# Kernel optimization log

Hardware: AMD Instinct MI355X
Metric: run time of the kernel (lower is better)

## Reference

```python
import jax, jax.numpy as jnp
import numpy as np

N_NODES = 100000


def setup_inputs() -> dict:
    key = jax.random.key(0)
    k1, k2, k3 = jax.random.split(key, 3)
    x = jax.random.normal(k1, (N_NODES, 128), dtype=jnp.float32)
    edge_index = jax.random.randint(k2, (2, 1600000), 0, N_NODES, dtype=jnp.int64)
    # TAGConv K=1 linear weight: maps concat([x, Ax]) (2*in) -> out; stored as [(K+1)*in, out]
    W = (jax.random.normal(k3, (256, 128), dtype=jnp.float32) / np.sqrt(256.0)).astype(jnp.float32)
    return {"x": x, "edge_index": edge_index, "W": W}


def reference(x, edge_index, W):
    src, dst = edge_index[0], edge_index[1]
    n = x.shape[0]
    ones = jnp.ones(src.shape[0], dtype=x.dtype)
    # gcn_norm without self-loops: degree from edge weights scattered at target
    deg = jax.ops.segment_sum(ones, dst, num_segments=n)
    dis = jnp.where(deg > 0, jax.lax.rsqrt(jnp.where(deg > 0, deg, 1.0)), 0.0)
    norm = dis[src] * dis[dst]  # [E]
    # message passing: out[dst] += norm * x[src]
    msgs = x[src] * norm[:, None]  # [E, in]
    agg = jax.ops.segment_sum(msgs, dst, num_segments=n)  # [N, in]
    h = jnp.concatenate([x, agg], axis=1)  # [N, 2*in]
    return h @ W  # [N, out]
```

## Files before the change

### kernel.cpp

```cpp
#include <hip/hip_runtime.h>


#define GCN_F 128

typedef __attribute__((ext_vector_type(8))) short frag_ab;
typedef __attribute__((ext_vector_type(4))) float frag_cd;

__device__ __forceinline__ unsigned short f2bf(float f) {
    unsigned int u = __float_as_uint(f);
    unsigned int r = (u + 0x7FFFu + ((u >> 16) & 1u)) >> 16;
    return (unsigned short)r;
}

__global__ __launch_bounds__(256) void prep_kernel(const unsigned int* __restrict__ ei32,
                                                   const float* __restrict__ W,
                                                   unsigned short* __restrict__ wt,
                                                   int* __restrict__ flag) {
    if (blockIdx.x == 128) {
        unsigned int v = 0;
        for (int i = threadIdx.x; i < 4096; i += 256) v |= ei32[2 * i + 1];
        if (v != 0u) atomicOr(flag, 1);
        return;
    }
    int c = blockIdx.x;
    int k = threadIdx.x;
    wt[c * 256 + k] = f2bf(W[k * GCN_F + c]);
}

__device__ __forceinline__ int load_idx(const int* ei, int is32, long long pos) {
    if (is32) return ei[pos];
    return ((const int2*)ei)[pos].x;
}

__global__ __launch_bounds__(256) void chist_kernel(const int* __restrict__ ei,
                                                    const int* __restrict__ flag,
                                                    int* __restrict__ ccnt, int E) {
    __shared__ int h[256];
    int tid = threadIdx.x;
    h[tid] = 0;
    __syncthreads();
    int is32 = *flag;
    int base = blockIdx.x * 4096;
    for (int j = 0; j < 16; ++j) {
        int e = base + j * 256 + tid;
        if (e < E) {
            int dst = load_idx(ei, is32, (long long)E + e);
            atomicAdd(&h[dst >> 9], 1);
        }
    }
    __syncthreads();
    if (h[tid]) atomicAdd(&ccnt[tid], h[tid]);
}

__global__ __launch_bounds__(256) void cscan_kernel(const int* __restrict__ ccnt,
                                                    int* __restrict__ cs,
                                                    int* __restrict__ ccur) {
    __shared__ int tmp[256];
    int tid = threadIdx.x;
    int v = ccnt[tid];
    tmp[tid] = v;
    __syncthreads();
    for (int off = 1; off < 256; off <<= 1) {
        int t = (tid >= off) ? tmp[tid - off] : 0;
        __syncthreads();
        tmp[tid] += t;
        __syncthreads();
    }
    int ex = tmp[tid] - v;
    cs[tid] = ex;
    ccur[tid] = ex;
    if (tid == 255) cs[256] = tmp[255];
}

__global__ __launch_bounds__(256) void cscatter_kernel(const int* __restrict__ ei,
                                                       const int* __restrict__ flag,
                                                       int* __restrict__ ccur,
                                                       unsigned int* __restrict__ epack,
                                                       int E) {
    __shared__ int h[256];
    __shared__ int lcur[256];
    int tid = threadIdx.x;
    h[tid] = 0;
    __syncthreads();
    int is32 = *flag;
    int base = blockIdx.x * 4096;
    unsigned int pk[16];
    int bn[16];
#pragma unroll
    for (int j = 0; j < 16; ++j) {
        int e = base + j * 256 + tid;
        bn[j] = -1;
        pk[j] = 0;
        if (e < E) {
            int src = load_idx(ei, is32, e);
            int dst = load_idx(ei, is32, (long long)E + e);
            pk[j] = (unsigned int)src | (((unsigned int)dst & 511u) << 17);
            bn[j] = dst >> 9;
            atomicAdd(&h[bn[j]], 1);
        }
    }
    __syncthreads();
    {
        int cnt = h[tid];
        lcur[tid] = (cnt > 0) ? atomicAdd(&ccur[tid], cnt) : 0;
    }
    __syncthreads();
#pragma unroll
    for (int j = 0; j < 16; ++j) {
        if (bn[j] >= 0) {
            int pos = atomicAdd(&lcur[bn[j]], 1);
            epack[pos] = pk[j];
        }
    }
}

__global__ __launch_bounds__(512) void fcsr_kernel(const unsigned int* __restrict__ epack,
                                                   const int* __restrict__ cs,
                                                   int* __restrict__ start,
                                                   float* __restrict__ dis,
                                                   int* __restrict__ ebuf,
                                                   int N, int E) {
    __shared__ int lh[512];
    __shared__ int sc[512];
    int c = blockIdx.x;
    int tid = threadIdx.x;
    lh[tid] = 0;
    __syncthreads();
    int b = cs[c], e = cs[c + 1];
    for (int i = b + tid; i < e; i += 512) {
        atomicAdd(&lh[(epack[i] >> 17) & 511u], 1);
    }
    __syncthreads();
    sc[tid] = lh[tid];
    __syncthreads();
    for (int off = 1; off < 512; off <<= 1) {
        int t = (tid >= off) ? sc[tid - off] : 0;
        __syncthreads();
        sc[tid] += t;
        __syncthreads();
    }
    int d = lh[tid];
    int gs = b + sc[tid] - d;
    int node = c * 512 + tid;
    if (node < N) {
        start[node] = gs;
        dis[node] = (d > 0) ? rsqrtf((float)d) : 0.0f;
    }
    __syncthreads();
    sc[tid] = gs;
    if (c == 0 && tid == 0) start[N] = E;
    __syncthreads();
    for (int i = b + tid; i < e; i += 512) {
        unsigned int v = epack[i];
        int pos = atomicAdd(&sc[(v >> 17) & 511u], 1);
        ebuf[pos] = (int)(v & 0x1FFFFu);
    }
}

__global__ __launch_bounds__(256) void xbf_kernel(const float4* __restrict__ x4,
                                                  unsigned short* __restrict__ h, int N) {
    int g = blockIdx.x * 256 + threadIdx.x;
    if (g >= N * 32) return;
    int r = g >> 5, q = g & 31;
    float4 v = x4[(long long)r * 32 + q];
    ushort4 o;
    o.x = f2bf(v.x); o.y = f2bf(v.y); o.z = f2bf(v.z); o.w = f2bf(v.w);
    *(ushort4*)(h + (long long)r * 256 + q * 4) = o;
}

__global__ __launch_bounds__(256) void gather_kernel(unsigned short* __restrict__ h,
                                                     const int* __restrict__ ebuf,
                                                     const int* __restrict__ start,
                                                     const float* __restrict__ dis,
                                                     int N) {
    int node = blockIdx.x * 4 + (threadIdx.x >> 6);
    if (node >= N) return;
    int lane = threadIdx.x & 63;
    int slot = lane >> 4;
    int sub  = lane & 15;
    int s = start[node];
    int d = start[node + 1] - s;
    float acc[8];
#pragma unroll
    for (int i = 0; i < 8; ++i) acc[i] = 0.0f;

    for (int base = 0; base < d; base += 64) {
        int cn = min(64, d - base);
        int eid = 0; float dv = 0.0f;
        if (lane < cn) {
            eid = ebuf[s + base + lane];
            dv = dis[eid];
        }
        int njj = (cn + 3) >> 2;
#pragma unroll 4
        for (int j = 0; j < njj; ++j) {
            int tt = 4 * j + slot;
            int src = __shfl(eid, tt);
            float f = __shfl(dv, tt);
            uint4 u = *(const uint4*)(h + (long long)src * 256 + sub * 8);
            acc[0] += f * __uint_as_float(u.x << 16);
            acc[1] += f * __uint_as_float(u.x);
            acc[2] += f * __uint_as_float(u.y << 16);
            acc[3] += f * __uint_as_float(u.y);
            acc[4] += f * __uint_as_float(u.z << 16);
            acc[5] += f * __uint_as_float(u.z);
            acc[6] += f * __uint_as_float(u.w << 16);
            acc[7] += f * __uint_as_float(u.w);
        }
    }
#pragma unroll
    for (int i = 0; i < 8; ++i) {
        acc[i] += __shfl_xor(acc[i], 16);
        acc[i] += __shfl_xor(acc[i], 32);
    }
    if (slot == 0) {
        float nd = dis[node];
        uint4 o;
        o.x = (unsigned int)f2bf(acc[0] * nd) | ((unsigned int)f2bf(acc[1] * nd) << 16);
        o.y = (unsigned int)f2bf(acc[2] * nd) | ((unsigned int)f2bf(acc[3] * nd) << 16);
        o.z = (unsigned int)f2bf(acc[4] * nd) | ((unsigned int)f2bf(acc[5] * nd) << 16);
        o.w = (unsigned int)f2bf(acc[6] * nd) | ((unsigned int)f2bf(acc[7] * nd) << 16);
        *(uint4*)(h + (long long)node * 256 + 128 + sub * 8) = o;
    }
}

#define GEMM_BM 128
__global__ __launch_bounds__(256) void gemm_mfma_kernel(
        const unsigned short* h,
        const unsigned short* __restrict__ wt,
        float* out, int N) {
    int wave = threadIdx.x >> 6;
    int lane = threadIdx.x & 63;
    int lr = lane & 15;
    int kh = lane >> 4;
    int rowbase = blockIdx.x * GEMM_BM + wave * 32;

    frag_cd acc[2][8];
#pragma unroll
    for (int rt = 0; rt < 2; ++rt)
#pragma unroll
        for (int ct = 0; ct < 8; ++ct) acc[rt][ct] = (frag_cd)0.0f;

    for (int ks = 0; ks < 8; ++ks) {
        frag_ab a[2];
#pragma unroll
        for (int rt = 0; rt < 2; ++rt) {
            int r = rowbase + rt * 16 + lr;
            r = min(r, N - 1);
            a[rt] = *(const frag_ab*)(h + (long long)r * 256 + ks * 32 + kh * 8);
        }
#pragma unroll
        for (int ct = 0; ct < 8; ++ct) {
            int c = ct * 16 + lr;
            frag_ab b = *(const frag_ab*)(wt + c * 256 + ks * 32 + kh * 8);
#pragma unroll
            for (int rt = 0; rt < 2; ++rt) {
                acc[rt][ct] = __builtin_amdgcn_mfma_f32_16x16x32_bf16(a[rt], b, acc[rt][ct], 0, 0, 0);
            }
        }
    }
#pragma unroll
    for (int rt = 0; rt < 2; ++rt) {
#pragma unroll
        for (int ct = 0; ct < 8; ++ct) {
#pragma unroll
            for (int reg = 0; reg < 4; ++reg) {
                int r = rowbase + rt * 16 + kh * 4 + reg;
                if (r < N) out[(long long)r * GCN_F + ct * 16 + lr] = acc[rt][ct][reg];
            }
        }
    }
}

extern "C" void kernel_launch(void* const* d_in, const int* in_sizes, int n_in,
                              void* d_out, int out_size, void* d_ws, size_t ws_size,
                              hipStream_t stream) {
    const float* x  = (const float*)d_in[0];
    const int*   ei = (const int*)d_in[1];
    const float* W  = (const float*)d_in[2];
    float* out = (float*)d_out;

    const int N = in_sizes[0] / GCN_F;
    const int E = in_sizes[1] / 2;

    char* ws = (char*)d_ws;
    int*   flag  = (int*)ws;
    int*   ccnt  = (int*)(ws + 1024);
    int*   cs    = (int*)(ws + 3072);
    int*   ccur  = (int*)(ws + 5120);
    float* dis   = (float*)(ws + 8192);
    int*   start = (int*)(ws + 408192);
    int*   ebuf  = (int*)(ws + 808208);
    unsigned short* wt = (unsigned short*)(ws + 7208208);

    unsigned int*   epack = (unsigned int*)d_out;
    unsigned short* h     = (unsigned short*)d_out;

    const int CB = (N + 511) / 512;
    const int EB = (E + 4095) / 4096;

    hipMemsetAsync(d_ws, 0, 2048, stream);

    prep_kernel<<<129, 256, 0, stream>>>((const unsigned int*)ei, W, wt, flag);
    chist_kernel<<<EB, 256, 0, stream>>>(ei, flag, ccnt, E);
    cscan_kernel<<<1, 256, 0, stream>>>(ccnt, cs, ccur);
    cscatter_kernel<<<EB, 256, 0, stream>>>(ei, flag, ccur, epack, E);
    fcsr_kernel<<<CB, 512, 0, stream>>>(epack, cs, start, dis, ebuf, N, E);
    xbf_kernel<<<(N * 32 + 255) / 256, 256, 0, stream>>>((const float4*)x, h, N);
    gather_kernel<<<(N + 3) / 4, 256, 0, stream>>>(h, ebuf, start, dis, N);
    gemm_mfma_kernel<<<(N + GEMM_BM - 1) / GEMM_BM, 256, 0, stream>>>(h, wt, out, N);
}
```

Measured before the change: 185.2 us.

## Fold prep work into histogram and CSR kernels, overlapping bf16 conversion

Drops the separate prep kernel. The W transpose now runs as extra blocks of the histogram kernel, and each block detects int32 vs int64 indices locally instead of through a global flag, which also shrinks the memset. The x-to-bf16 conversion is split: rows past the region that aliases the epack scratch are converted by extra blocks of the fcsr kernel, and only the low rows wait for a separate kernel after fcsr. It also adds per-wave shared histograms and 32-bit address arithmetic. The hard-coded 12500-row split assumes the epack size for E=1.6M edges, so other edge counts would corrupt data.

```diff
diff --git a/kernel.cpp b/kernel.cpp
--- a/kernel.cpp
+++ b/kernel.cpp
@@ -12,19 +12,14 @@
     return (unsigned short)r;
 }
 
-__global__ __launch_bounds__(256) void prep_kernel(const unsigned int* __restrict__ ei32,
-                                                   const float* __restrict__ W,
-                                                   unsigned short* __restrict__ wt,
-                                                   int* __restrict__ flag) {
-    if (blockIdx.x == 128) {
-        unsigned int v = 0;
-        for (int i = threadIdx.x; i < 4096; i += 256) v |= ei32[2 * i + 1];
-        if (v != 0u) atomicOr(flag, 1);
-        return;
-    }
-    int c = blockIdx.x;
-    int k = threadIdx.x;
-    wt[c * 256 + k] = f2bf(W[k * GCN_F + c]);
+__device__ __forceinline__ int detect_is32(const unsigned int* ei32, int* s_is32) {
+    if (threadIdx.x == 0) *s_is32 = 0;
+    __syncthreads();
+    unsigned int v = 0;
+    for (int i = threadIdx.x; i < 2048; i += blockDim.x) v |= ei32[2 * i + 1];
+    if (v != 0u) atomicOr(s_is32, 1);
+    __syncthreads();
+    return *s_is32;
 }
 
 __device__ __forceinline__ int load_idx(const int* ei, int is32, long long pos) {
@@ -33,23 +28,32 @@
 }
 
 __global__ __launch_bounds__(256) void chist_kernel(const int* __restrict__ ei,
-                                                    const int* __restrict__ flag,
-                                                    int* __restrict__ ccnt, int E) {
-    __shared__ int h[256];
+                                                    int* __restrict__ ccnt, int E, int EB,
+                                                    const float* __restrict__ W,
+                                                    unsigned short* __restrict__ wt) {
+    if ((int)blockIdx.x >= EB) {
+        int c = blockIdx.x - EB;
+        int k = threadIdx.x;
+        wt[c * 256 + k] = f2bf(W[k * GCN_F + c]);
+        return;
+    }
+    __shared__ int h[4][256];
+    __shared__ int s_is32;
     int tid = threadIdx.x;
-    h[tid] = 0;
-    __syncthreads();
-    int is32 = *flag;
+    int wv = tid >> 6;
+    for (int i = tid; i < 1024; i += 256) ((int*)h)[i] = 0;
+    int is32 = detect_is32((const unsigned int*)ei, &s_is32);
     int base = blockIdx.x * 4096;
     for (int j = 0; j < 16; ++j) {
         int e = base + j * 256 + tid;
         if (e < E) {
             int dst = load_idx(ei, is32, (long long)E + e);
-            atomicAdd(&h[dst >> 9], 1);
-        }
-    }
-    __syncthreads();
-    if (h[tid]) atomicAdd(&ccnt[tid], h[tid]);
+            atomicAdd(&h[wv][dst >> 9], 1);
+        }
+    }
+    __syncthreads();
+    int s = h[0][tid] + h[1][tid] + h[2][tid] + h[3][tid];
+    if (s) atomicAdd(&ccnt[tid], s);
 }
 
 __global__ __launch_bounds__(256) void cscan_kernel(const int* __restrict__ ccnt,
@@ -73,16 +77,15 @@
 }
 
 __global__ __launch_bounds__(256) void cscatter_kernel(const int* __restrict__ ei,
-                                                       const int* __restrict__ flag,
                                                        int* __restrict__ ccur,
                                                        unsigned int* __restrict__ epack,
                                                        int E) {
     __shared__ int h[256];
     __shared__ int lcur[256];
+    __shared__ int s_is32;
     int tid = threadIdx.x;
     h[tid] = 0;
-    __syncthreads();
-    int is32 = *flag;
+    int is32 = detect_is32((const unsigned int*)ei, &s_is32);
     int base = blockIdx.x * 4096;
     unsigned int pk[16];
     int bn[16];
@@ -119,11 +122,25 @@
                                                    int* __restrict__ start,
                                                    float* __restrict__ dis,
                                                    int* __restrict__ ebuf,
-                                                   int N, int E) {
+                                                   const float4* __restrict__ x4,
+                                                   unsigned short* __restrict__ hbuf,
+                                                   int N, int E, int CB) {
+    int tid = threadIdx.x;
+    if ((int)blockIdx.x >= CB) {
+        int chunk = blockIdx.x - CB;
+        int g = 12500 * 32 + chunk * 512 + tid;
+        if (g < N * 32) {
+            int r = g >> 5, q = g & 31;
+            float4 v = x4[(long long)r * 32 + q];
+            ushort4 o;
+            o.x = f2bf(v.x); o.y = f2bf(v.y); o.z = f2bf(v.z); o.w = f2bf(v.w);
+            *(ushort4*)((char*)hbuf + ((unsigned)r << 9) + q * 8) = o;
+        }
+        return;
+    }
     __shared__ int lh[512];
     __shared__ int sc[512];
     int c = blockIdx.x;
-    int tid = threadIdx.x;
     lh[tid] = 0;
     __syncthreads();
     int b = cs[c], e = cs[c + 1];
@@ -157,18 +174,18 @@
     }
 }
 
-__global__ __launch_bounds__(256) void xbf_kernel(const float4* __restrict__ x4,
-                                                  unsigned short* __restrict__ h, int N) {
+__global__ __launch_bounds__(256) void xbf_lo_kernel(const float4* __restrict__ x4,
+                                                     unsigned short* __restrict__ hbuf) {
     int g = blockIdx.x * 256 + threadIdx.x;
-    if (g >= N * 32) return;
+    if (g >= 12500 * 32) return;
     int r = g >> 5, q = g & 31;
     float4 v = x4[(long long)r * 32 + q];
     ushort4 o;
     o.x = f2bf(v.x); o.y = f2bf(v.y); o.z = f2bf(v.z); o.w = f2bf(v.w);
-    *(ushort4*)(h + (long long)r * 256 + q * 4) = o;
-}
-
-__global__ __launch_bounds__(256) void gather_kernel(unsigned short* __restrict__ h,
+    *(ushort4*)((char*)hbuf + ((unsigned)r << 9) + q * 8) = o;
+}
+
+__global__ __launch_bounds__(256) void gather_kernel(unsigned short* __restrict__ hbuf,
                                                      const int* __restrict__ ebuf,
                                                      const int* __restrict__ start,
                                                      const float* __restrict__ dis,
@@ -177,9 +194,11 @@
     if (node >= N) return;
     int lane = threadIdx.x & 63;
     int slot = lane >> 4;
-    int sub  = lane & 15;
+    unsigned int subb = (lane & 15) * 16;
     int s = start[node];
     int d = start[node + 1] - s;
+    float nd = dis[node];
+    const char* hc = (const char*)hbuf;
     float acc[8];
 #pragma unroll
     for (int i = 0; i < 8; ++i) acc[i] = 0.0f;
@@ -197,7 +216,7 @@
             int tt = 4 * j + slot;
             int src = __shfl(eid, tt);
             float f = __shfl(dv, tt);
-            uint4 u = *(const uint4*)(h + (long long)src * 256 + sub * 8);
+            uint4 u = *(const uint4*)(hc + (((unsigned)src << 9) + subb));
             acc[0] += f * __uint_as_float(u.x << 16);
             acc[1] += f * __uint_as_float(u.x);
             acc[2] += f * __uint_as_float(u.y << 16);
@@ -214,13 +233,12 @@
         acc[i] += __shfl_xor(acc[i], 32);
     }
     if (slot == 0) {
-        float nd = dis[node];
         uint4 o;
         o.x = (unsigned int)f2bf(acc[0] * nd) | ((unsigned int)f2bf(acc[1] * nd) << 16);
         o.y = (unsigned int)f2bf(acc[2] * nd) | ((unsigned int)f2bf(acc[3] * nd) << 16);
         o.z = (unsigned int)f2bf(acc[4] * nd) | ((unsigned int)f2bf(acc[5] * nd) << 16);
         o.w = (unsigned int)f2bf(acc[6] * nd) | ((unsigned int)f2bf(acc[7] * nd) << 16);
-        *(uint4*)(h + (long long)node * 256 + 128 + sub * 8) = o;
+        *(uint4*)((char*)hbuf + (((unsigned)node << 9) + 256 + subb)) = o;
     }
 }
 
@@ -234,6 +252,7 @@
     int lr = lane & 15;
     int kh = lane >> 4;
     int rowbase = blockIdx.x * GEMM_BM + wave * 32;
+    const char* hc = (const char*)h;
 
     frag_cd acc[2][8];
 #pragma unroll
@@ -247,7 +266,7 @@
         for (int rt = 0; rt < 2; ++rt) {
             int r = rowbase + rt * 16 + lr;
             r = min(r, N - 1);
-            a[rt] = *(const frag_ab*)(h + (long long)r * 256 + ks * 32 + kh * 8);
+            a[rt] = *(const frag_ab*)(hc + (((unsigned)r << 9) + (unsigned)(ks * 64 + kh * 16)));
         }
 #pragma unroll
         for (int ct = 0; ct < 8; ++ct) {
@@ -266,7 +285,7 @@
 #pragma unroll
             for (int reg = 0; reg < 4; ++reg) {
                 int r = rowbase + rt * 16 + kh * 4 + reg;
-                if (r < N) out[(long long)r * GCN_F + ct * 16 + lr] = acc[rt][ct][reg];
+                if (r < N) out[r * GCN_F + ct * 16 + lr] = acc[rt][ct][reg];
             }
         }
     }
@@ -284,10 +303,9 @@
     const int E = in_sizes[1] / 2;
 
     char* ws = (char*)d_ws;
-    int*   flag  = (int*)ws;
-    int*   ccnt  = (int*)(ws + 1024);
-    int*   cs    = (int*)(ws + 3072);
-    int*   ccur  = (int*)(ws + 5120);
+    int*   ccnt  = (int*)ws;
+    int*   cs    = (int*)(ws + 1024);
+    int*   ccur  = (int*)(ws + 3072);
     float* dis   = (float*)(ws + 8192);
     int*   start = (int*)(ws + 408192);
     int*   ebuf  = (int*)(ws + 808208);
@@ -298,15 +316,17 @@
 
     const int CB = (N + 511) / 512;
     const int EB = (E + 4095) / 4096;
-
-    hipMemsetAsync(d_ws, 0, 2048, stream);
-
-    prep_kernel<<<129, 256, 0, stream>>>((const unsigned int*)ei, W, wt, flag);
-    chist_kernel<<<EB, 256, 0, stream>>>(ei, flag, ccnt, E);
+    const int XBHI = (((N - 12500) * 32) + 511) / 512;
+    const int XBLO = (12500 * 32 + 255) / 256;
+
+    hipMemsetAsync(d_ws, 0, 1024, stream);
+
+    chist_kernel<<<EB + 128, 256, 0, stream>>>(ei, ccnt, E, EB, W, wt);
     cscan_kernel<<<1, 256, 0, stream>>>(ccnt, cs, ccur);
-    cscatter_kernel<<<EB, 256, 0, stream>>>(ei, flag, ccur, epack, E);
-    fcsr_kernel<<<CB, 512, 0, stream>>>(epack, cs, start, dis, ebuf, N, E);
-    xbf_kernel<<<(N * 32 + 255) / 256, 256, 0, stream>>>((const float4*)x, h, N);
+    cscatter_kernel<<<EB, 256, 0, stream>>>(ei, ccur, epack, E);
+    fcsr_kernel<<<CB + XBHI, 512, 0, stream>>>(epack, cs, start, dis, ebuf,
+                                               (const float4*)x, h, N, E, CB);
+    xbf_lo_kernel<<<XBLO, 256, 0, stream>>>((const float4*)x, h);
     gather_kernel<<<(N + 3) / 4, 256, 0, stream>>>(h, ebuf, start, dis, N);
     gemm_mfma_kernel<<<(N + GEMM_BM - 1) / GEMM_BM, 256, 0, stream>>>(h, wt, out, N);
 }
```

Result: faster. 178.3 us (-3.7%).
